# Kernel optimization log

Hardware: AMD Instinct MI355X
Metric: run time of the kernel (lower is better)

The kernel has to match this reference:

```python
import jax, jax.numpy as jnp
import numpy as np

BATCH, T, H, S, P, NH = 4, 2048, 1024, 64, 64, 8
HD = H // NH

def setup_inputs() -> dict:
    key = jax.random.key(0)
    ks = jax.random.split(key, 16)
    sH = 1.0 / np.sqrt(H)
    d = {}
    d["builder_state"] = jax.random.normal(ks[0], (BATCH, T, H), jnp.float32)
    d["base_state"] = jax.random.normal(ks[1], (BATCH, T, H), jnp.float32)
    d["input_ids"] = jax.random.randint(ks[2], (BATCH, T), 0, 32000)
    d["program_probs"] = jax.random.uniform(ks[3], (BATCH, T, P), jnp.float32)
    # SSM params (scaled from raw randn for numerical stability of the 2048-step recurrence)
    d["A"] = jax.random.normal(ks[4], (S, S), jnp.float32) * (0.5 / np.sqrt(S))
    d["Bmat"] = jax.random.normal(ks[5], (H, S), jnp.float32) * sH
    d["Cmat"] = jax.random.normal(ks[6], (S, H), jnp.float32) * (1.0 / np.sqrt(S))
    d["W_in"] = jax.random.normal(ks[7], (H, H), jnp.float32) * sH
    d["b_in"] = jnp.zeros((H,), jnp.float32)
    d["W_qkv"] = jax.random.normal(ks[8], (3 * H, H), jnp.float32) * sH
    d["b_qkv"] = jnp.zeros((3 * H,), jnp.float32)
    d["W_o"] = jax.random.normal(ks[9], (H, H), jnp.float32) * sH
    d["b_o"] = jnp.zeros((H,), jnp.float32)
    d["W_prog"] = jax.random.normal(ks[10], (H, P), jnp.float32) * (1.0 / np.sqrt(P))
    d["b_prog"] = jnp.zeros((H,), jnp.float32)
    d["g1"] = jnp.ones((H,), jnp.float32); d["beta1"] = jnp.zeros((H,), jnp.float32)
    d["g2"] = jnp.ones((H,), jnp.float32); d["beta2"] = jnp.zeros((H,), jnp.float32)
    return d

def _layernorm(x, g, b):
    mu = jnp.mean(x, axis=-1, keepdims=True)
    var = jnp.mean((x - mu) ** 2, axis=-1, keepdims=True)
    return (x - mu) * jax.lax.rsqrt(var + 1e-5) * g + b

def _mha(q_in, kv_in, W_qkv, b_qkv, W_o, b_o):
    Wq, Wk, Wv = jnp.split(W_qkv, 3, axis=0)
    bq, bk, bv = jnp.split(b_qkv, 3, axis=0)
    def heads(x, W, b):  # [B,T,H] -> [B,NH,T,HD]
        y = x @ W.T + b
        return y.reshape(y.shape[0], y.shape[1], NH, HD).transpose(0, 2, 1, 3)
    q, k, v = heads(q_in, Wq, bq), heads(kv_in, Wk, bk), heads(kv_in, Wv, bv)
    scores = jnp.einsum('bhqd,bhkd->bhqk', q, k) * (1.0 / np.sqrt(HD))
    attn = jax.nn.softmax(scores, axis=-1)
    out = jnp.einsum('bhqk,bhkd->bhqd', attn, v)
    out = out.transpose(0, 2, 1, 3).reshape(q_in.shape)
    return out @ W_o.T + b_o

def reference(builder_state, base_state, input_ids, program_probs,
              A, Bmat, Cmat, W_in, b_in, W_qkv, b_qkv, W_o, b_o,
              W_prog, b_prog, g1, beta1, g2, beta2):
    # cross-attention sublayer (norm1 shared between builder and base states)
    residual = builder_state
    x = _layernorm(builder_state, g1, beta1)
    base_n = _layernorm(base_state, g1, beta1)
    x = residual + _mha(x, base_n, W_qkv, b_qkv, W_o, b_o)
    # SSM sublayer: state_{t} = silu(A @ state_{t-1}) + B^T u_t ; y_t = state_t @ C
    residual = x
    xn = _layernorm(x, g2, beta2)
    U = (xn @ W_in.T + b_in) @ Bmat            # [B,T,S] precomputed input drive
    def step(s, u_t):                           # s: [B,S], u_t: [B,S]
        s = jax.nn.silu(s @ A.T) + u_t
        return s, s
    _, states = jax.lax.scan(step, jnp.zeros((builder_state.shape[0], S), U.dtype),
                             U.transpose(1, 0, 2))  # states: [T,B,S]
    ssm_out = jnp.einsum('tbs,sh->bth', states, Cmat)
    x = residual + ssm_out
    # program modulation
    mod = program_probs.mean(axis=1) @ W_prog.T + b_prog   # [B,H]
    return x + mod[:, None, :]
```

## Files before the change

kernel.cpp:

```cpp
#include <hip/hip_runtime.h>
#include <cstdint>
#include <cstddef>

typedef unsigned short u16;
typedef short bf16x8 __attribute__((ext_vector_type(8)));
typedef float f32x4 __attribute__((ext_vector_type(4)));
typedef u16 u16x4 __attribute__((ext_vector_type(4)));
typedef u16 u16x8 __attribute__((ext_vector_type(8)));

#define DEVFN static __device__ __forceinline__

DEVFN u16 f32_to_bf16(float f){
  unsigned u = __float_as_uint(f);
  u += 0x7fffu + ((u >> 16) & 1u);
  return (u16)(u >> 16);
}

DEVFN f32x4 mfma16(bf16x8 a, bf16x8 b, f32x4 c){
  return __builtin_amdgcn_mfma_f32_16x16x32_bf16(a, b, c, 0, 0, 0);
}

__global__ void cast4_kernel(const float4* __restrict__ src, u16x4* __restrict__ dst, int n4){
  for (int i = blockIdx.x*blockDim.x + threadIdx.x; i < n4; i += gridDim.x*blockDim.x){
    float4 v = src[i];
    u16x4 o; o[0]=f32_to_bf16(v.x); o[1]=f32_to_bf16(v.y); o[2]=f32_to_bf16(v.z); o[3]=f32_to_bf16(v.w);
    dst[i] = o;
  }
}

__global__ void tcast_kernel(const float* __restrict__ Cm, u16* __restrict__ CmT){
  int i = blockIdx.x*256 + threadIdx.x;
  int h = i >> 6, s = i & 63;
  CmT[i] = f32_to_bf16(Cm[s*1024 + h]);
}

__global__ __launch_bounds__(256,1) void wcomb_kernel(const float* __restrict__ W_in,
    const float* __restrict__ Bm, u16* __restrict__ WcT){
  const int kl = threadIdx.x & 63, sl = threadIdx.x >> 6;
  const int k = ((blockIdx.x & 15) << 6) + kl;
  const int s = ((blockIdx.x >> 4) << 2) + sl;
  float a = 0.f;
#pragma unroll 8
  for (int jj = 0; jj < 1024; jj++) a = fmaf(W_in[jj*1024 + k], Bm[jj*64 + s], a);
  WcT[s*1024 + k] = f32_to_bf16(a);
}

__global__ void ubias_kernel(const float* __restrict__ b_in, const float* __restrict__ Bm,
                             float* __restrict__ ub){
  const int s = threadIdx.x;
  float a = 0.f;
  for (int jj = 0; jj < 1024; jj++) a = fmaf(b_in[jj], Bm[jj*64 + s], a);
  ub[s] = a;
}

__global__ __launch_bounds__(256,1) void ln_bf16_kernel(
    const float* __restrict__ src, u16* __restrict__ dst,
    const float* __restrict__ g, const float* __restrict__ beta)
{
  const int row = blockIdx.x, t = threadIdx.x;
  const float4 v = ((const float4*)(src + (size_t)row*1024))[t];
  float s1 = v.x+v.y+v.z+v.w;
  float s2 = v.x*v.x+v.y*v.y+v.z*v.z+v.w*v.w;
#pragma unroll
  for (int off = 32; off > 0; off >>= 1){ s1 += __shfl_xor(s1, off); s2 += __shfl_xor(s2, off); }
  __shared__ float w1[4], w2[4];
  if ((t & 63) == 0){ w1[t>>6] = s1; w2[t>>6] = s2; }
  __syncthreads();
  s1 = (w1[0]+w1[1])+(w1[2]+w1[3]);
  s2 = (w2[0]+w2[1])+(w2[2]+w2[3]);
  const float mean = s1*(1.f/1024.f);
  const float var  = s2*(1.f/1024.f) - mean*mean;
  const float rstd = rsqrtf(var + 1e-5f);
  const float4 gv = ((const float4*)g)[t];
  const float4 bv = ((const float4*)beta)[t];
  u16x4 o;
  o[0] = f32_to_bf16((v.x-mean)*rstd*gv.x + bv.x);
  o[1] = f32_to_bf16((v.y-mean)*rstd*gv.y + bv.y);
  o[2] = f32_to_bf16((v.z-mean)*rstd*gv.z + bv.z);
  o[3] = f32_to_bf16((v.w-mean)*rstd*gv.w + bv.w);
  *(u16x4*)&dst[(size_t)row*1024 + t*4] = o;
}

template<int BM,int BN,int WM,int WN,int MT,int NT,int EPI>
__global__ __launch_bounds__(256,1) void gemm_bt(
    const u16* __restrict__ Ag, const u16* __restrict__ Bg,
    void* __restrict__ Cout, const float* __restrict__ bias,
    const float* __restrict__ resid, const float* __restrict__ modv,
    int M, int N, int K)
{
  static_assert(BM == WM*MT*16 && BN == WN*NT*16 && WM*WN == 4, "tile config");
  __shared__ u16 As[BM*40];
  __shared__ u16 Bs[BN*40];
  const int t = threadIdx.x;
  const int lane = t & 63, wave = t >> 6;
  const int wm = wave / WN, wn = wave % WN;
  const int lrow = lane & 15, lq = lane >> 4;
  const int m0 = blockIdx.y * BM, n0 = blockIdx.x * BN;

  f32x4 acc[MT][NT];
#pragma unroll
  for (int i = 0; i < MT; i++)
#pragma unroll
    for (int j = 0; j < NT; j++){ acc[i][j][0]=0.f; acc[i][j][1]=0.f; acc[i][j][2]=0.f; acc[i][j][3]=0.f; }

  for (int kt = 0; kt < K; kt += 32){
#pragma unroll
    for (int i = 0; i < BM/64; i++){
      int idx = t + i*256;
      int r = idx >> 2, c = (idx & 3) << 3;
      *(u16x8*)&As[r*40 + c] = *(const u16x8*)&Ag[(size_t)(m0 + r)*K + kt + c];
    }
#pragma unroll
    for (int i = 0; i < BN/64; i++){
      int idx = t + i*256;
      int r = idx >> 2, c = (idx & 3) << 3;
      *(u16x8*)&Bs[r*40 + c] = *(const u16x8*)&Bg[(size_t)(n0 + r)*K + kt + c];
    }
    __syncthreads();
    bf16x8 af[MT], bfr[NT];
#pragma unroll
    for (int mt = 0; mt < MT; mt++)
      af[mt] = *(const bf16x8*)&As[(wm*MT*16 + mt*16 + lrow)*40 + lq*8];
#pragma unroll
    for (int nt = 0; nt < NT; nt++)
      bfr[nt] = *(const bf16x8*)&Bs[(wn*NT*16 + nt*16 + lrow)*40 + lq*8];
#pragma unroll
    for (int mt = 0; mt < MT; mt++)
#pragma unroll
      for (int nt = 0; nt < NT; nt++)
        acc[mt][nt] = mfma16(af[mt], bfr[nt], acc[mt][nt]);
    __syncthreads();
  }
  const int rb = m0 + wm*MT*16;
  const int cb = n0 + wn*NT*16;
#pragma unroll
  for (int mt = 0; mt < MT; mt++){
#pragma unroll
    for (int nt = 0; nt < NT; nt++){
#pragma unroll
      for (int r = 0; r < 4; r++){
        int row = rb + mt*16 + lq*4 + r;
        int col = cb + nt*16 + lrow;
        float v = acc[mt][nt][r];
        if (EPI & 2) v += bias[col];
        if (EPI & 4) v += resid[(size_t)row*N + col];
        if (EPI & 8) v += modv[(row >> 11)*1024 + col];
        if (EPI & 1) ((u16*)Cout)[(size_t)row*N + col] = f32_to_bf16(v);
        else         ((float*)Cout)[(size_t)row*N + col] = v;
      }
    }
  }
}

__global__ __launch_bounds__(256,1) void flash_attn(
    const u16* __restrict__ Qb, const u16* __restrict__ KVb, u16* __restrict__ Ob)
{
  __shared__ u16 Ks[64*128];
  __shared__ unsigned Vt2[128*34];
  __shared__ u16 Ps[4][16*68];
  const int t = threadIdx.x;
  const int lane = t & 63, wave = t >> 6;
  const int lrow = lane & 15, lq = lane >> 4;
  const int b = blockIdx.y >> 3, h = blockIdx.y & 7;
  const int q0 = blockIdx.x * 64;
  const float C1 = 0.08838834764831845f * 1.4426950408889634f;

  bf16x8 qf[4];
  {
    int grow = b*2048 + q0 + wave*16 + lrow;
#pragma unroll
    for (int ks = 0; ks < 4; ks++)
      qf[ks] = *(const bf16x8*)&Qb[(size_t)grow*1024 + h*128 + ks*32 + lq*8];
  }
  float lsum[4] = {0.f,0.f,0.f,0.f};
  f32x4 Oa[8];
#pragma unroll
  for (int i = 0; i < 8; i++){ Oa[i][0]=0.f; Oa[i][1]=0.f; Oa[i][2]=0.f; Oa[i][3]=0.f; }

  const int key_k = t >> 2, cg = t & 3;
  const int kp = t & 31, dg = t >> 5;

  for (int kt = 0; kt < 32; kt++){
    __syncthreads();
    {
      const u16* kpg = &KVb[(size_t)(b*2048 + kt*64 + key_k)*2048 + h*128];
#pragma unroll
      for (int i = 0; i < 4; i++){
        int ch = cg*4 + i;
        int ph = ch ^ (key_k & 7);
        *(u16x8*)&Ks[key_k*128 + ph*8] = *(const u16x8*)&kpg[ch*8];
      }
      const u16* vg = &KVb[(size_t)(b*2048 + kt*64 + kp*2)*2048 + h*128 + 1024 + dg*16];
      u16x8 v0a = *(const u16x8*)&vg[0];
      u16x8 v0b = *(const u16x8*)&vg[8];
      u16x8 v1a = *(const u16x8*)&vg[2048];
      u16x8 v1b = *(const u16x8*)&vg[2048+8];
#pragma unroll
      for (int jj = 0; jj < 8; jj++){
        Vt2[(dg*16+jj)*34 + kp]     = (unsigned)v0a[jj] | ((unsigned)v1a[jj] << 16);
        Vt2[(dg*16+8+jj)*34 + kp]   = (unsigned)v0b[jj] | ((unsigned)v1b[jj] << 16);
      }
    }
    __syncthreads();

    f32x4 sacc[4];
#pragma unroll
    for (int nt = 0; nt < 4; nt++){
      f32x4 a; a[0]=0.f; a[1]=0.f; a[2]=0.f; a[3]=0.f;
#pragma unroll
      for (int ks = 0; ks < 4; ks++){
        int ph = (ks*4 + lq) ^ (lrow & 7);
        bf16x8 kf = *(const bf16x8*)&Ks[(nt*16+lrow)*128 + ph*8];
        a = mfma16(qf[ks], kf, a);
      }
      sacc[nt] = a;
    }
#pragma unroll
    for (int nt = 0; nt < 4; nt++)
#pragma unroll
      for (int r = 0; r < 4; r++){
        float p = exp2f(sacc[nt][r]*C1);
        lsum[r] += p;
        Ps[wave][(lq*4+r)*68 + nt*16 + lrow] = f32_to_bf16(p);
      }
#pragma unroll
    for (int ks2 = 0; ks2 < 2; ks2++){
      bf16x8 pa;
      ((u16x4*)&pa)[0] = *(const u16x4*)&Ps[wave][lrow*68 + ks2*32 + lq*8];
      ((u16x4*)&pa)[1] = *(const u16x4*)&Ps[wave][lrow*68 + ks2*32 + lq*8 + 4];
#pragma unroll
      for (int nt2 = 0; nt2 < 8; nt2++){
        bf16x8 vf;
        int dwoff = (nt2*16+lrow)*34 + ks2*16 + lq*4;
        ((uint2*)&vf)[0] = *(const uint2*)&Vt2[dwoff];
        ((uint2*)&vf)[1] = *(const uint2*)&Vt2[dwoff+2];
        Oa[nt2] = mfma16(pa, vf, Oa[nt2]);
      }
    }
  }
#pragma unroll
  for (int r = 0; r < 4; r++){
#pragma unroll
    for (int off = 1; off < 16; off <<= 1) lsum[r] += __shfl_xor(lsum[r], off);
  }
  float inv[4];
#pragma unroll
  for (int r = 0; r < 4; r++) inv[r] = 1.0f / lsum[r];
  const int growb = b*2048 + q0 + wave*16;
#pragma unroll
  for (int nt2 = 0; nt2 < 8; nt2++)
#pragma unroll
    for (int r = 0; r < 4; r++){
      float o = Oa[nt2][r]*inv[r];
      Ob[(size_t)(growb + lq*4 + r)*1024 + h*128 + nt2*16 + lrow] = f32_to_bf16(o);
    }
}

__global__ __launch_bounds__(64,1) void scan_chunk_kernel(
    const float* __restrict__ U, const float* __restrict__ A, u16* __restrict__ S)
{
  const int b = blockIdx.y, c = blockIdx.x, j = threadIdx.x;
  float Ar[64];
#pragma unroll
  for (int k = 0; k < 64; k++) Ar[k] = A[j*64 + k];
  const float* Ub = U + (size_t)b*2048*64;
  u16* Sb = S + (size_t)b*2048*64;
  const int tout = c*32;
  const int tend = tout + 32;
  int t0 = tout - 48; if (t0 < 0) t0 = 0;
  __shared__ float sbuf[2][64];
  sbuf[0][j] = 0.f;
  __syncthreads();
  float unext = Ub[t0*64 + j];
  const float NLOG2E = -1.4426950408889634f;
  for (int t = t0; t < tend; t++){
    const int cur = (t - t0) & 1;
    f32x4 sv[16];
#pragma unroll
    for (int r = 0; r < 16; r++) sv[r] = *((const f32x4*)&sbuf[cur][r*4]);
    float u = unext;
    int tn = t + 1; if (tn >= tend) tn = tend - 1;
    unext = Ub[tn*64 + j];
    float a0=0.f, a1=0.f, a2=0.f, a3=0.f;
#pragma unroll
    for (int r = 0; r < 16; r++){
      a0 = fmaf(Ar[4*r+0], sv[r][0], a0);
      a1 = fmaf(Ar[4*r+1], sv[r][1], a1);
      a2 = fmaf(Ar[4*r+2], sv[r][2], a2);
      a3 = fmaf(Ar[4*r+3], sv[r][3], a3);
    }
    float y = (a0+a1)+(a2+a3);
    float e = exp2f(y*NLOG2E);
    float s = fmaf(y, __builtin_amdgcn_rcpf(1.f + e), u);
    sbuf[cur^1][j] = s;
    if (t >= tout) Sb[t*64 + j] = f32_to_bf16(s);
  }
}

__global__ __launch_bounds__(256,1) void pmean1_kernel(const float* __restrict__ pp,
                                                       float* __restrict__ partial){
  const int c = blockIdx.x, b = blockIdx.y, t = threadIdx.x;
  const int p = t & 63, g = t >> 6;
  const float* basep = pp + (size_t)b*2048*64 + (size_t)c*64*64;
  float s = 0.f;
#pragma unroll
  for (int i = g*16; i < g*16 + 16; i++) s += basep[i*64 + p];
  __shared__ float red[256];
  red[t] = s;
  __syncthreads();
  if (t < 64) partial[(b*32 + c)*64 + t] = (red[t] + red[64+t]) + (red[128+t] + red[192+t]);
}

__global__ void pmean2_kernel(const float* __restrict__ partial, float* __restrict__ pm){
  const int b = blockIdx.x, p = threadIdx.x;
  float s = 0.f;
#pragma unroll
  for (int c = 0; c < 32; c++) s += partial[(b*32 + c)*64 + p];
  pm[b*64 + p] = s * (1.f/2048.f);
}

__global__ void mod_kernel(const float* __restrict__ pm, const float* __restrict__ Wp,
                           const float* __restrict__ bp, float* __restrict__ mo){
  const int i = blockIdx.x*256 + threadIdx.x;
  const int b = i >> 10, hc = i & 1023;
  float s = bp[hc];
#pragma unroll 8
  for (int p = 0; p < 64; p++) s = fmaf(pm[b*64+p], Wp[hc*64+p], s);
  mo[i] = s;
}

extern "C" void kernel_launch(void* const* d_in, const int* in_sizes, int n_in,
                              void* d_out, int out_size, void* d_ws, size_t ws_size,
                              hipStream_t stream)
{
  (void)in_sizes; (void)n_in; (void)out_size; (void)ws_size;
  const float* builder = (const float*)d_in[0];
  const float* base    = (const float*)d_in[1];
  const float* pp      = (const float*)d_in[3];
  const float* Amat    = (const float*)d_in[4];
  const float* Bmat    = (const float*)d_in[5];
  const float* Cmat    = (const float*)d_in[6];
  const float* W_in    = (const float*)d_in[7];
  const float* b_in    = (const float*)d_in[8];
  const float* W_qkv   = (const float*)d_in[9];
  const float* b_qkv   = (const float*)d_in[10];
  const float* W_o     = (const float*)d_in[11];
  const float* b_o     = (const float*)d_in[12];
  const float* W_prog  = (const float*)d_in[13];
  const float* b_prog  = (const float*)d_in[14];
  const float* g1      = (const float*)d_in[15];
  const float* beta1   = (const float*)d_in[16];
  const float* g2      = (const float*)d_in[17];
  const float* beta2   = (const float*)d_in[18];
  float* out = (float*)d_out;

  char* ws = (char*)d_ws;
  const size_t MB = (size_t)1 << 20;
  u16*   Qb   = (u16*)  (ws + 0*MB);
  u16*   KVb  = (u16*)  (ws + 16*MB);
  float* Xf   = (float*)(ws + 48*MB);
  u16*   QN   = (u16*)  (ws + 80*MB);
  u16*   KVN  = (u16*)  (ws + 96*MB);
  u16*   Wq16 = (u16*)  (ws + 112*MB);
  u16*   Wo16 = (u16*)  (ws + 118*MB);
  u16*   WcT  = (u16*)  (ws + 120*MB);
  u16*   CmT  = (u16*)  (ws + 120*MB + 256*1024);
  float* Uf   = (float*)(ws + 121*MB);
  u16*   Sb   = (u16*)  (ws + 123*MB);
  float* ub   = (float*)(ws + 124*MB);
  float* pmv  = (float*)(ws + 124*MB + 4096);
  float* modv = (float*)(ws + 124*MB + 8192);
  float* ppart= (float*)(ws + 124*MB + 32768);

  cast4_kernel<<<1024,256,0,stream>>>((const float4*)W_qkv, (u16x4*)Wq16, 3145728/4);
  cast4_kernel<<<1024,256,0,stream>>>((const float4*)W_o,   (u16x4*)Wo16, 1048576/4);
  tcast_kernel<<<256,256,0,stream>>>(Cmat, CmT);
  wcomb_kernel<<<256,256,0,stream>>>(W_in, Bmat, WcT);
  ubias_kernel<<<1,64,0,stream>>>(b_in, Bmat, ub);

  ln_bf16_kernel<<<8192,256,0,stream>>>(builder, QN,  g1, beta1);
  ln_bf16_kernel<<<8192,256,0,stream>>>(base,    KVN, g1, beta1);

  gemm_bt<128,128,2,2,4,4,3><<<dim3(8,64),256,0,stream>>>(QN,  Wq16,              Qb,  b_qkv,      nullptr, nullptr, 8192,1024,1024);
  gemm_bt<128,128,2,2,4,4,3><<<dim3(16,64),256,0,stream>>>(KVN, Wq16 + 1024*1024, KVb, b_qkv+1024, nullptr, nullptr, 8192,2048,1024);

  flash_attn<<<dim3(32,32),256,0,stream>>>(Qb, KVb, QN);

  gemm_bt<128,128,2,2,4,4,6><<<dim3(8,64),256,0,stream>>>(QN, Wo16, Xf, b_o, builder, nullptr, 8192,1024,1024);

  ln_bf16_kernel<<<8192,256,0,stream>>>(Xf, KVN, g2, beta2);

  gemm_bt<64,64,2,2,2,2,2><<<dim3(1,128),256,0,stream>>>(KVN, WcT, Uf, ub, nullptr, nullptr, 8192,64,1024);

  scan_chunk_kernel<<<dim3(64,4),64,0,stream>>>(Uf, Amat, Sb);

  pmean1_kernel<<<dim3(32,4),256,0,stream>>>(pp, ppart);
  pmean2_kernel<<<4,64,0,stream>>>(ppart, pmv);
  mod_kernel<<<16,256,0,stream>>>(pmv, W_prog, b_prog, modv);

  gemm_bt<128,128,2,2,4,4,12><<<dim3(8,64),256,0,stream>>>(Sb, CmT, out, nullptr, Xf, modv, 8192,1024,64);
}
```

Baseline: 635.9 us.

## Double query rows per wave in flash attention to reuse K/V tiles

```diff
diff --git a/kernel.cpp b/kernel.cpp
--- a/kernel.cpp
+++ b/kernel.cpp
@@ -157,25 +157,28 @@
 {
   __shared__ u16 Ks[64*128];
   __shared__ unsigned Vt2[128*34];
-  __shared__ u16 Ps[4][16*68];
+  __shared__ u16 Ps[4][32*68];
   const int t = threadIdx.x;
   const int lane = t & 63, wave = t >> 6;
   const int lrow = lane & 15, lq = lane >> 4;
-  const int b = blockIdx.y >> 3, h = blockIdx.y & 7;
-  const int q0 = blockIdx.x * 64;
+  const int b = blockIdx.x >> 3, h = blockIdx.x & 7;
+  const int q0 = blockIdx.y * 128;
   const float C1 = 0.08838834764831845f * 1.4426950408889634f;
 
-  bf16x8 qf[4];
-  {
-    int grow = b*2048 + q0 + wave*16 + lrow;
+  bf16x8 qf[2][4];
+#pragma unroll
+  for (int mt = 0; mt < 2; mt++){
+    int grow = b*2048 + q0 + wave*32 + mt*16 + lrow;
 #pragma unroll
     for (int ks = 0; ks < 4; ks++)
-      qf[ks] = *(const bf16x8*)&Qb[(size_t)grow*1024 + h*128 + ks*32 + lq*8];
-  }
-  float lsum[4] = {0.f,0.f,0.f,0.f};
-  f32x4 Oa[8];
-#pragma unroll
-  for (int i = 0; i < 8; i++){ Oa[i][0]=0.f; Oa[i][1]=0.f; Oa[i][2]=0.f; Oa[i][3]=0.f; }
+      qf[mt][ks] = *(const bf16x8*)&Qb[(size_t)grow*1024 + h*128 + ks*32 + lq*8];
+  }
+  float lsum[2][4] = {{0.f,0.f,0.f,0.f},{0.f,0.f,0.f,0.f}};
+  f32x4 Oa[2][8];
+#pragma unroll
+  for (int mt = 0; mt < 2; mt++)
+#pragma unroll
+    for (int i = 0; i < 8; i++){ Oa[mt][i][0]=0.f; Oa[mt][i][1]=0.f; Oa[mt][i][2]=0.f; Oa[mt][i][3]=0.f; }
 
   const int key_k = t >> 2, cg = t & 3;
   const int kp = t & 31, dg = t >> 5;
@@ -203,57 +206,68 @@
     }
     __syncthreads();
 
-    f32x4 sacc[4];
+    f32x4 sacc[2][4];
 #pragma unroll
     for (int nt = 0; nt < 4; nt++){
-      f32x4 a; a[0]=0.f; a[1]=0.f; a[2]=0.f; a[3]=0.f;
+      f32x4 a0; a0[0]=0.f; a0[1]=0.f; a0[2]=0.f; a0[3]=0.f;
+      f32x4 a1 = a0;
 #pragma unroll
       for (int ks = 0; ks < 4; ks++){
         int ph = (ks*4 + lq) ^ (lrow & 7);
         bf16x8 kf = *(const bf16x8*)&Ks[(nt*16+lrow)*128 + ph*8];
-        a = mfma16(qf[ks], kf, a);
-      }
-      sacc[nt] = a;
-    }
-#pragma unroll
-    for (int nt = 0; nt < 4; nt++)
-#pragma unroll
-      for (int r = 0; r < 4; r++){
-        float p = exp2f(sacc[nt][r]*C1);
-        lsum[r] += p;
-        Ps[wave][(lq*4+r)*68 + nt*16 + lrow] = f32_to_bf16(p);
-      }
+        a0 = mfma16(qf[0][ks], kf, a0);
+        a1 = mfma16(qf[1][ks], kf, a1);
+      }
+      sacc[0][nt] = a0; sacc[1][nt] = a1;
+    }
+#pragma unroll
+    for (int mt = 0; mt < 2; mt++)
+#pragma unroll
+      for (int nt = 0; nt < 4; nt++)
+#pragma unroll
+        for (int r = 0; r < 4; r++){
+          float p = exp2f(sacc[mt][nt][r]*C1);
+          lsum[mt][r] += p;
+          Ps[wave][(mt*16 + lq*4 + r)*68 + nt*16 + lrow] = f32_to_bf16(p);
+        }
 #pragma unroll
     for (int ks2 = 0; ks2 < 2; ks2++){
-      bf16x8 pa;
-      ((u16x4*)&pa)[0] = *(const u16x4*)&Ps[wave][lrow*68 + ks2*32 + lq*8];
-      ((u16x4*)&pa)[1] = *(const u16x4*)&Ps[wave][lrow*68 + ks2*32 + lq*8 + 4];
+      bf16x8 pa[2];
+#pragma unroll
+      for (int mt = 0; mt < 2; mt++){
+        ((u16x4*)&pa[mt])[0] = *(const u16x4*)&Ps[wave][(mt*16 + lrow)*68 + ks2*32 + lq*8];
+        ((u16x4*)&pa[mt])[1] = *(const u16x4*)&Ps[wave][(mt*16 + lrow)*68 + ks2*32 + lq*8 + 4];
+      }
 #pragma unroll
       for (int nt2 = 0; nt2 < 8; nt2++){
         bf16x8 vf;
         int dwoff = (nt2*16+lrow)*34 + ks2*16 + lq*4;
         ((uint2*)&vf)[0] = *(const uint2*)&Vt2[dwoff];
         ((uint2*)&vf)[1] = *(const uint2*)&Vt2[dwoff+2];
-        Oa[nt2] = mfma16(pa, vf, Oa[nt2]);
-      }
-    }
-  }
-#pragma unroll
-  for (int r = 0; r < 4; r++){
-#pragma unroll
-    for (int off = 1; off < 16; off <<= 1) lsum[r] += __shfl_xor(lsum[r], off);
-  }
-  float inv[4];
-#pragma unroll
-  for (int r = 0; r < 4; r++) inv[r] = 1.0f / lsum[r];
-  const int growb = b*2048 + q0 + wave*16;
-#pragma unroll
-  for (int nt2 = 0; nt2 < 8; nt2++)
+        Oa[0][nt2] = mfma16(pa[0], vf, Oa[0][nt2]);
+        Oa[1][nt2] = mfma16(pa[1], vf, Oa[1][nt2]);
+      }
+    }
+  }
+#pragma unroll
+  for (int mt = 0; mt < 2; mt++)
 #pragma unroll
     for (int r = 0; r < 4; r++){
-      float o = Oa[nt2][r]*inv[r];
-      Ob[(size_t)(growb + lq*4 + r)*1024 + h*128 + nt2*16 + lrow] = f32_to_bf16(o);
-    }
+#pragma unroll
+      for (int off = 1; off < 16; off <<= 1) lsum[mt][r] += __shfl_xor(lsum[mt][r], off);
+      lsum[mt][r] = 1.0f / lsum[mt][r];
+    }
+#pragma unroll
+  for (int mt = 0; mt < 2; mt++){
+    const int growb = b*2048 + q0 + wave*32 + mt*16;
+#pragma unroll
+    for (int nt2 = 0; nt2 < 8; nt2++)
+#pragma unroll
+      for (int r = 0; r < 4; r++){
+        float o = Oa[mt][nt2][r]*lsum[mt][r];
+        Ob[(size_t)(growb + lq*4 + r)*1024 + h*128 + nt2*16 + lrow] = f32_to_bf16(o);
+      }
+  }
 }
 
 __global__ __launch_bounds__(64,1) void scan_chunk_kernel(
@@ -384,7 +398,7 @@
   gemm_bt<128,128,2,2,4,4,3><<<dim3(8,64),256,0,stream>>>(QN,  Wq16,              Qb,  b_qkv,      nullptr, nullptr, 8192,1024,1024);
   gemm_bt<128,128,2,2,4,4,3><<<dim3(16,64),256,0,stream>>>(KVN, Wq16 + 1024*1024, KVb, b_qkv+1024, nullptr, nullptr, 8192,2048,1024);
 
-  flash_attn<<<dim3(32,32),256,0,stream>>>(Qb, KVb, QN);
+  flash_attn<<<dim3(32,16),256,0,stream>>>(Qb, KVb, QN);
 
   gemm_bt<128,128,2,2,4,4,6><<<dim3(8,64),256,0,stream>>>(QN, Wo16, Xf, b_o, builder, nullptr, 8192,1024,1024);
 
```

New measurement: 665.4 us. 4.6% more time.
